# Kernel optimization log

Measured on AMD Instinct MI355X. Metric: run time of the kernel, lower is better.

Reference implementation:

```python
import jax, jax.numpy as jnp
import numpy as np

N_NODE = 50000   # item vocab
D = 100          # embed_dim / hidden_size
N = 49152        # total nodes across all sessions
E = 98304        # edges
B = 4096         # sessions
STDV = 1.0 / np.sqrt(D)


def setup_inputs() -> dict:
    key = jax.random.key(0)
    ks = jax.random.split(key, 20)
    # 1-based item ids, shape [N,1] as in data.x
    x = jax.random.randint(ks[0], (N, 1), 1, N_NODE + 1, dtype=jnp.int32)
    edge_index = jax.random.randint(ks[1], (2, E), 0, N, dtype=jnp.int32)
    # sorted session ids; every session appears at least once (split/nodes[-1] needs non-empty)
    base = jnp.arange(B, dtype=jnp.int32)
    extra = jax.random.randint(ks[2], (N - B,), 0, B, dtype=jnp.int32)
    batch = jnp.sort(jnp.concatenate([base, extra]))

    def u(k, shape):
        return jax.random.uniform(k, shape, minval=-STDV, maxval=STDV, dtype=jnp.float32)

    return {
        "x": x, "edge_index": edge_index, "batch": batch, "num_sessions": B,
        "emb": u(ks[3], (N_NODE, D)),
        "conv_w": u(ks[4], (D, D)),          # GatedGraphConv weight[0]
        "gru_w_ih": u(ks[5], (3 * D, D)),
        "gru_w_hh": u(ks[6], (3 * D, D)),
        "gru_b_ih": u(ks[7], (3 * D,)),
        "gru_b_hh": u(ks[8], (3 * D,)),
        "q_w": u(ks[9], (1, D)), "q_b": u(ks[10], (1,)),
        "w2_w": u(ks[11], (D, D)), "w2_b": u(ks[12], (D,)),
        "w3_w": u(ks[13], (D, D)), "w3_b": u(ks[14], (D,)),
        "w4_w": u(ks[15], (D, 3 * D)), "w4_b": u(ks[16], (D,)),
    }


def _forward(x, edge_index, batch, num_sessions, emb, conv_w,
             gru_w_ih, gru_w_hh, gru_b_ih, gru_b_hh,
             q_w, q_b, w2_w, w2_b, w3_w, w3_b, w4_w, w4_b):
    ids = x[:, 0] - 1                              # data.x - 1
    h0 = emb[ids]                                  # [N, D]

    # GatedGraphConv(num_layers=1): m = x @ W; aggregate sum src->dst; GRUCell update
    src, dst = edge_index[0], edge_index[1]
    m = h0 @ conv_w                                # [N, D]
    agg = jnp.zeros_like(h0).at[dst].add(m[src])   # segment-sum aggregation
    gi = agg @ gru_w_ih.T + gru_b_ih               # [N, 3D]
    gh = h0 @ gru_w_hh.T + gru_b_hh
    i_r, i_z, i_n = jnp.split(gi, 3, axis=1)
    h_r, h_z, h_n = jnp.split(gh, 3, axis=1)
    r = jax.nn.sigmoid(i_r + h_r)
    z = jax.nn.sigmoid(i_z + h_z)
    n = jnp.tanh(i_n + r * h_n)
    xh = jax.nn.relu((1.0 - z) * n + z * h0)       # F.relu(Conv(x, edge_index))

    # last node per session (batch is sorted, sessions non-empty)
    counts = jax.ops.segment_sum(jnp.ones_like(batch), batch, num_segments=num_sessions)
    last_idx = jnp.cumsum(counts) - 1
    v_n = xh[last_idx]                             # [B, D]

    # get_scores: per-session softmax(v_n . nodes) weighted sum -> S_s
    logits = jnp.sum(xh * v_n[batch], axis=1)      # [N]
    mx = jax.ops.segment_max(logits, batch, num_segments=num_sessions)
    p = jnp.exp(logits - mx[batch])
    denom = jax.ops.segment_sum(p, batch, num_segments=num_sessions)
    score = p / denom[batch]                       # [N]
    S_s = jax.ops.segment_sum(score[:, None] * xh, batch, num_segments=num_sessions)

    # sigmoid-gated attention pooling -> S_g
    gate = jax.nn.sigmoid(xh @ w2_w.T + w2_b + v_n[batch] @ w3_w.T + w3_b)
    alpha = gate @ q_w.T + q_b                     # [N, 1]
    S_g = jax.ops.segment_sum(alpha * xh, batch, num_segments=num_sessions)

    S = jnp.concatenate([S_s, S_g, v_n], axis=1) @ w4_w.T + w4_b  # [B, D]
    y_hat = S @ emb.T                              # [B, n_node]
    return y_hat


def reference(x, edge_index, batch, num_sessions, emb, conv_w,
              gru_w_ih, gru_w_hh, gru_b_ih, gru_b_hh,
              q_w, q_b, w2_w, w2_b, w3_w, w3_b, w4_w, w4_b):
    return _forward(x, edge_index, batch, num_sessions, emb, conv_w,
                    gru_w_ih, gru_w_hh, gru_b_ih, gru_b_hh,
                    q_w, q_b, w2_w, w2_b, w3_w, w3_b, w4_w, w4_b)
```

## Files before the change

### kernel.cpp

```cpp
#include <hip/hip_runtime.h>
#include <math.h>

#define DDIM 100
#define PFD  4
#define NTG  4
#define XS   108

using short8 = __attribute__((ext_vector_type(8))) short;
using f32x4  = __attribute__((ext_vector_type(4))) float;


__device__ __forceinline__ float sigm(float x) { return 1.f / (1.f + expf(-x)); }

__device__ __forceinline__ f32x4 mfma16(short8 a, short8 b, f32x4 c) {
  return __builtin_amdgcn_mfma_f32_16x16x32_bf16(a, b, c, 0, 0, 0);
}

__device__ __forceinline__ void gld_lds16(const void* g, void* l) {
  __builtin_amdgcn_global_load_lds(
      (const __attribute__((address_space(1))) void*)g,
      (__attribute__((address_space(3))) void*)l, 16, 0, 0);
}

__device__ __forceinline__ void bf16split(float v, short& h, short& l) {
  unsigned u = __float_as_uint(v);
  unsigned hb = (u + 0x7fffu + ((u >> 16) & 1u)) & 0xffff0000u;
  float res = v - __uint_as_float(hb);
  unsigned u2 = __float_as_uint(res);
  h = (short)(hb >> 16);
  l = (short)((u2 + 0x7fffu + ((u2 >> 16) & 1u)) >> 16);
}

__device__ __forceinline__ short bf16hi(float v) {
  unsigned u = __float_as_uint(v);
  return (short)((u + 0x7fffu + ((u >> 16) & 1u)) >> 16);
}

__global__ __launch_bounds__(256) void k_wc(const float* __restrict__ w_ih,
                                            const float* __restrict__ conv_w,
                                            float* __restrict__ Wc) {
  __shared__ float cwT[100 * 100];
  const int tid = threadIdx.x;
  for (int idx = tid; idx < 10000; idx += 256) {
    int k = idx / 100, t = idx - k * 100;
    cwT[t * 100 + k] = conv_w[idx];
  }
  __syncthreads();
  const int cBase = blockIdx.x * 25;
  for (int o = tid; o < 25 * 100; o += 256) {
    int c = cBase + o / 100;
    int k = o - (o / 100) * 100;
    const float* wr = w_ih + (size_t)c * 100;
    float acc = 0.f;
    for (int t = 0; t < 100; ++t) acc = fmaf(wr[t], cwT[t * 100 + k], acc);
    Wc[(size_t)c * 100 + k] = acc;
  }
}

__global__ void k_packAll(const int* __restrict__ x, const float* __restrict__ emb,
                          const int* __restrict__ batch, const float* __restrict__ Wc,
                          const float* __restrict__ w_hh, const float* __restrict__ w2,
                          const float* __restrict__ w3,
                          short8* __restrict__ Bhi, short8* __restrict__ Blo,
                          short8* __restrict__ Whi,
                          float4* __restrict__ h0, int* __restrict__ last_idx,
                          int NNODE, int NT, int N) {
  int gid = blockIdx.x * 256 + threadIdx.x;
  const int embN = NT * 4 * 64;
  const int wN = 8 * 7 * 4 * 64;
  if (gid < embN) {
    int lane = gid & 63;
    int kt = (gid >> 6) & 3;
    int rt = gid >> 8;
    int r = rt * 16 + (lane & 15);
    if (r >= NNODE) r = NNODE - 1;
    int k0 = kt * 32 + (lane >> 4) * 8;
    float4 f0 = make_float4(0.f, 0.f, 0.f, 0.f);
    float4 f1 = make_float4(0.f, 0.f, 0.f, 0.f);
    if (k0 < 100)     f0 = *(const float4*)(emb + (size_t)r * DDIM + k0);
    if (k0 + 4 < 100) f1 = *(const float4*)(emb + (size_t)r * DDIM + k0 + 4);
    float v[8] = {f0.x, f0.y, f0.z, f0.w, f1.x, f1.y, f1.z, f1.w};
    short8 h, l;
#pragma unroll
    for (int j = 0; j < 8; ++j) {
      short hh, ll;
      bf16split(v[j], hh, ll);
      h[j] = hh; l[j] = ll;
    }
    Bhi[gid] = h;
    Blo[gid] = l;
  } else if (gid < embN + wN) {
    int wg = gid - embN;
    int lane = wg & 63;
    int kt = (wg >> 6) & 3;
    int snt = wg >> 8;
    int nt = snt % 7;
    int s = snt / 7;
    int d = nt * 16 + (lane & 15);
    int k0 = kt * 32 + (lane >> 4) * 8;
    short8 h;
#pragma unroll
    for (int j = 0; j < 8; ++j) {
      int k = k0 + j;
      float v = 0.f;
      if (d < 100 && k < 100) {
        if (s < 3) {
          v = Wc[(size_t)(s * 100 + d) * 100 + k];
        } else if (s < 6) {
          v = w_hh[(size_t)((s - 3) * 100 + d) * 100 + k];
        } else if (s == 6) {
          v = w2[(size_t)d * 100 + k];
        } else {
          v = w3[(size_t)d * 100 + k];
        }
      }
      h[j] = bf16hi(v);
    }
    Whi[wg] = h;
  } else {
    int i = gid - embN - wN;
    if (i < N * 25) {
      int node = i / 25, c = i - node * 25;
      h0[i] = *(const float4*)(emb + (size_t)(x[node] - 1) * DDIM + 4 * c);
    }
    if (i < N) {
      if (i == N - 1 || batch[i + 1] != batch[i]) last_idx[batch[i]] = i;
    }
  }
}

__global__ __launch_bounds__(512, 1) void k_aggregate(
    const int* __restrict__ ei, const float* __restrict__ h0,
    float* __restrict__ aggH, int E) {
  __shared__ float acc[256 * DDIM];
  const int tid = threadIdx.x;
  const int lane = tid & 63;
  const int wave = tid >> 6;
  const int r0 = blockIdx.x * 256;

  for (int idx = tid; idx < 256 * DDIM / 4; idx += 512)
    ((float4*)acc)[idx] = make_float4(0.f, 0.f, 0.f, 0.f);
  __syncthreads();

  const int per = E >> 3;
  const int base = wave * per;
  for (int it = 0; it < per; it += 256) {
    int e0 = base + it + lane * 4;
    int4 d4 = *(const int4*)(ei + E + e0);
    int4 s4 = *(const int4*)(ei + e0);
    int darr[4] = {d4.x, d4.y, d4.z, d4.w};
    int sarr[4] = {s4.x, s4.y, s4.z, s4.w};
#pragma unroll
    for (int j = 0; j < 4; ++j) {
      int dj = darr[j] - r0;
      bool match = (unsigned)dj < 256u;
      unsigned long long mask = __ballot(match);
      while (mask) {
        int bit = __ffsll(mask) - 1;
        mask &= mask - 1;
        int ds = __shfl(dj, bit, 64);
        int ss = __shfl(sarr[j], bit, 64);
        if (lane < 25) {
          float4 v = *(const float4*)(h0 + (size_t)ss * DDIM + 4 * lane);
          float* a = acc + ds * DDIM + 4 * lane;
          atomicAdd(a + 0, v.x); atomicAdd(a + 1, v.y);
          atomicAdd(a + 2, v.z); atomicAdd(a + 3, v.w);
        }
      }
    }
  }
  __syncthreads();
  float4* of = (float4*)(aggH + (size_t)r0 * DDIM);
  for (int idx = tid; idx < 256 * DDIM / 4; idx += 512)
    of[idx] = ((const float4*)acc)[idx];
}

__global__ __launch_bounds__(256) void k_session(
    const float* __restrict__ xh, const float* __restrict__ t2,
    const float* __restrict__ t3v,
    const float* __restrict__ q_w, const float* __restrict__ q_b,
    const int* __restrict__ last_idx, float* __restrict__ Scat, int B) {
  int sid = blockIdx.x * 4 + (threadIdx.x >> 6);
  if (sid >= B) return;
  const int lane = threadIdx.x & 63;
  const int g = lane >> 4;
  const int s = lane & 15;
  const int start = (sid == 0) ? 0 : last_idx[sid - 1] + 1;
  const int end = last_idx[sid];

  float vr[7], t3r[7], qr[7];
#pragma unroll
  for (int k = 0; k < 7; ++k) {
    int c = s + 16 * k;
    bool ok = c < DDIM;
    vr[k]  = ok ? xh[(size_t)end * DDIM + c] : 0.f;
    t3r[k] = ok ? t3v[(size_t)sid * DDIM + c] : 0.f;
    qr[k]  = ok ? q_w[c] : 0.f;
  }
  const float qb = q_b[0];

  float m = -INFINITY, den = 0.f;
  float ss[7] = {}, sg[7] = {};
  for (int i = start; i <= end; i += 4) {
    int ni = i + g;
    bool act = ni <= end;
    int nrow = act ? ni : end;
    float xv[7];
    float l = 0.f, ga = 0.f;
#pragma unroll
    for (int k = 0; k < 7; ++k) {
      int c = s + 16 * k;
      float x = (c < DDIM) ? xh[(size_t)nrow * DDIM + c] : 0.f;
      float tv = (c < DDIM) ? t2[(size_t)nrow * DDIM + c] : 0.f;
      xv[k] = x;
      l = fmaf(x, vr[k], l);
      ga = fmaf(qr[k], sigm(tv + t3r[k]), ga);
    }
#pragma unroll
    for (int o = 1; o <= 8; o <<= 1) {
      l += __shfl_xor(l, o, 64);
      ga += __shfl_xor(ga, o, 64);
    }
    float ls = act ? l : -INFINITY;
    float alpha = act ? (ga + qb) : 0.f;
    float mn = fmaxf(m, ls);
    float cf = (m == -INFINITY) ? 0.f : expf(m - mn);
    float p = act ? expf(ls - mn) : 0.f;
    den = den * cf + p;
#pragma unroll
    for (int k = 0; k < 7; ++k) {
      ss[k] = ss[k] * cf + p * xv[k];
      sg[k] = fmaf(alpha, xv[k], sg[k]);
    }
    m = mn;
  }
  float mAll = m;
  mAll = fmaxf(mAll, __shfl_xor(mAll, 16, 64));
  mAll = fmaxf(mAll, __shfl_xor(mAll, 32, 64));
  float sc = (m == -INFINITY) ? 0.f : expf(m - mAll);
  float dv = den * sc;
  dv += __shfl_xor(dv, 16, 64);
  dv += __shfl_xor(dv, 32, 64);
  float inv = 1.f / dv;
  float* Sc = Scat + (size_t)sid * 300;
#pragma unroll
  for (int k = 0; k < 7; ++k) {
    float sv = ss[k] * sc;
    float gv = sg[k];
    sv += __shfl_xor(sv, 16, 64);  sv += __shfl_xor(sv, 32, 64);
    gv += __shfl_xor(gv, 16, 64);  gv += __shfl_xor(gv, 32, 64);
    int c = s + 16 * k;
    if (g == 0 && c < DDIM) {
      Sc[c] = sv * inv;
      Sc[100 + c] = gv;
      Sc[200 + c] = vr[k];
    }
  }
}

__device__ __forceinline__ void load_afragsH(const float* __restrict__ A, int rowBase,
                                             int lane, short8 ah[4]) {
  int r = rowBase + (lane & 15);
  int g = lane >> 4;
#pragma unroll
  for (int kt = 0; kt < 4; ++kt) {
    int k0 = kt * 32 + g * 8;
    float4 f0 = make_float4(0.f, 0.f, 0.f, 0.f);
    float4 f1 = make_float4(0.f, 0.f, 0.f, 0.f);
    if (k0 < 100)     f0 = *(const float4*)(A + (size_t)r * DDIM + k0);
    if (k0 + 4 < 100) f1 = *(const float4*)(A + (size_t)r * DDIM + k0 + 4);
    short8 h;
    h[0] = bf16hi(f0.x); h[1] = bf16hi(f0.y); h[2] = bf16hi(f0.z); h[3] = bf16hi(f0.w);
    h[4] = bf16hi(f1.x); h[5] = bf16hi(f1.y); h[6] = bf16hi(f1.z); h[7] = bf16hi(f1.w);
    ah[kt] = h;
  }
}

__device__ __forceinline__ void load_afragsHg(const float* __restrict__ A,
                                              const int* __restrict__ idx, int base,
                                              int lane, short8 ah[4]) {
  int r = idx[base + (lane & 15)];
  int g = lane >> 4;
#pragma unroll
  for (int kt = 0; kt < 4; ++kt) {
    int k0 = kt * 32 + g * 8;
    float4 f0 = make_float4(0.f, 0.f, 0.f, 0.f);
    float4 f1 = make_float4(0.f, 0.f, 0.f, 0.f);
    if (k0 < 100)     f0 = *(const float4*)(A + (size_t)r * DDIM + k0);
    if (k0 + 4 < 100) f1 = *(const float4*)(A + (size_t)r * DDIM + k0 + 4);
    short8 h;
    h[0] = bf16hi(f0.x); h[1] = bf16hi(f0.y); h[2] = bf16hi(f0.z); h[3] = bf16hi(f0.w);
    h[4] = bf16hi(f1.x); h[5] = bf16hi(f1.y); h[6] = bf16hi(f1.z); h[7] = bf16hi(f1.w);
    ah[kt] = h;
  }
}

__global__ __launch_bounds__(256) void k_grufused(
    const float* __restrict__ aggH, const float* __restrict__ h0,
    const short8* __restrict__ Whi,
    const float* __restrict__ b_ih, const float* __restrict__ b_hh,
    const float* __restrict__ b2,
    float* __restrict__ xh, float* __restrict__ t2) {
  __shared__ float X[4 * 32 * XS];
  const int lane = threadIdx.x & 63;
  const int wave = threadIdx.x >> 6;
  const int rowBase = blockIdx.x * 128 + wave * 32;
  float* xs = &X[wave * 32 * XS];
  short8 aI0[4], aI1[4], aH0[4], aH1[4];
  load_afragsH(aggH, rowBase, lane, aI0);
  load_afragsH(aggH, rowBase + 16, lane, aI1);
  load_afragsH(h0, rowBase, lane, aH0);
  load_afragsH(h0, rowBase + 16, lane, aH1);
  const int c0 = lane & 15;
  const int r0 = (lane >> 4) * 4;

  for (int nt = 0; nt < 7; ++nt) {
    int d = nt * 16 + c0;
    f32x4 a0[6] = {};
    f32x4 a1[6] = {};
#pragma unroll
    for (int s = 0; s < 6; ++s) {
#pragma unroll
      for (int kt = 0; kt < 4; ++kt) {
        short8 w = Whi[(((size_t)s * 7 + nt) * 4 + kt) * 64 + lane];
        if (s < 3) {
          a0[s] = mfma16(aI0[kt], w, a0[s]);
          a1[s] = mfma16(aI1[kt], w, a1[s]);
        } else {
          a0[s] = mfma16(aH0[kt], w, a0[s]);
          a1[s] = mfma16(aH1[kt], w, a1[s]);
        }
      }
    }
    if (d < 100) {
      float bir = b_ih[d], biz = b_ih[100 + d], bin_ = b_ih[200 + d];
      float bhr = b_hh[d], bhz = b_hh[100 + d], bhn = b_hh[200 + d];
#pragma unroll
      for (int ri = 0; ri < 4; ++ri) {
        {
          int row = rowBase + r0 + ri;
          float r = sigm(a0[0][ri] + bir + a0[3][ri] + bhr);
          float z = sigm(a0[1][ri] + biz + a0[4][ri] + bhz);
          float n = tanhf(a0[2][ri] + bin_ + r * (a0[5][ri] + bhn));
          float h0v = h0[(size_t)row * DDIM + d];
          float v = (1.f - z) * n + z * h0v;
          xs[(r0 + ri) * XS + d] = v > 0.f ? v : 0.f;
        }
        {
          int row = rowBase + 16 + r0 + ri;
          float r = sigm(a1[0][ri] + bir + a1[3][ri] + bhr);
          float z = sigm(a1[1][ri] + biz + a1[4][ri] + bhz);
          float n = tanhf(a1[2][ri] + bin_ + r * (a1[5][ri] + bhn));
          float h0v = h0[(size_t)row * DDIM + d];
          float v = (1.f - z) * n + z * h0v;
          xs[(16 + r0 + ri) * XS + d] = v > 0.f ? v : 0.f;
        }
      }
    }
  }

  const int lr = lane / 25;
  const int lc4 = (lane - lr * 25) * 4;
  if (lane < 50) {
#pragma unroll
    for (int p = 0; p < 16; ++p) {
      int row = p * 2 + lr;
      f32x4 v = *(const f32x4*)&xs[row * XS + lc4];
      *(f32x4*)(xh + (size_t)(rowBase + row) * DDIM + lc4) = v;
    }
  }

  short8 xa0[4], xa1[4];
  {
    int r = lane & 15;
    int g = lane >> 4;
#pragma unroll
    for (int kt = 0; kt < 4; ++kt) {
      int k0 = kt * 32 + g * 8;
      short8 h0f, h1f;
#pragma unroll
      for (int j = 0; j < 8; ++j) {
        int k = k0 + j;
        float v0 = (k < 100) ? xs[r * XS + k] : 0.f;
        float v1 = (k < 100) ? xs[(16 + r) * XS + k] : 0.f;
        h0f[j] = bf16hi(v0);
        h1f[j] = bf16hi(v1);
      }
      xa0[kt] = h0f;
      xa1[kt] = h1f;
    }
  }

  for (int nt = 0; nt < 7; ++nt) {
    int d = nt * 16 + c0;
    f32x4 ac0 = {0.f, 0.f, 0.f, 0.f};
    f32x4 ac1 = {0.f, 0.f, 0.f, 0.f};
#pragma unroll
    for (int kt = 0; kt < 4; ++kt) {
      short8 w = Whi[(((size_t)6 * 7 + nt) * 4 + kt) * 64 + lane];
      ac0 = mfma16(xa0[kt], w, ac0);
      ac1 = mfma16(xa1[kt], w, ac1);
    }
    if (d < 100) {
      float b = b2[d];
#pragma unroll
      for (int ri = 0; ri < 4; ++ri) {
        xs[(r0 + ri) * XS + d] = ac0[ri] + b;
        xs[(16 + r0 + ri) * XS + d] = ac1[ri] + b;
      }
    }
  }
  if (lane < 50) {
#pragma unroll
    for (int p = 0; p < 16; ++p) {
      int row = p * 2 + lr;
      f32x4 v = *(const f32x4*)&xs[row * XS + lc4];
      *(f32x4*)(t2 + (size_t)(rowBase + row) * DDIM + lc4) = v;
    }
  }
}

__global__ __launch_bounds__(256) void k_t3v(
    const float* __restrict__ xh, const short8* __restrict__ Whi,
    const float* __restrict__ b3, const int* __restrict__ lastI,
    float* __restrict__ t3v) {
  const int lane = threadIdx.x & 63;
  const int wave = threadIdx.x >> 6;
  const int rowBase = blockIdx.x * 128 + wave * 32;
  short8 a0[4], a1[4];
  load_afragsHg(xh, lastI, rowBase, lane, a0);
  load_afragsHg(xh, lastI, rowBase + 16, lane, a1);
  const int c0 = lane & 15;
  const int r0 = (lane >> 4) * 4;

  for (int nt = 0; nt < 7; ++nt) {
    int d = nt * 16 + c0;
    f32x4 ac0 = {0.f, 0.f, 0.f, 0.f};
    f32x4 ac1 = {0.f, 0.f, 0.f, 0.f};
#pragma unroll
    for (int kt = 0; kt < 4; ++kt) {
      short8 w = Whi[(((size_t)7 * 7 + nt) * 4 + kt) * 64 + lane];
      ac0 = mfma16(a0[kt], w, ac0);
      ac1 = mfma16(a1[kt], w, ac1);
    }
    if (d < 100) {
      float b = b3[d];
#pragma unroll
      for (int ri = 0; ri < 4; ++ri) {
        t3v[(size_t)(rowBase + r0 + ri) * DDIM + d] = ac0[ri] + b;
        t3v[(size_t)(rowBase + 16 + r0 + ri) * DDIM + d] = ac1[ri] + b;
      }
    }
  }
}

__global__ __launch_bounds__(256, 2) void k_gemmS(
    const float* __restrict__ A, const float* __restrict__ Bm,
    const float* __restrict__ bias, short* __restrict__ Ph, short* __restrict__ Pl,
    int M) {
  __shared__ float4 As4[25 * 128];
  __shared__ float4 Bs4[25 * 64];
  const int m0 = blockIdx.y * 128;
  const int n0 = blockIdx.x * 64;
  const int t = threadIdx.x;
  const int tx = t & 15;
  const int ty = t >> 4;
  float acc[8][4] = {};

  for (int kt = 0; kt < 300; kt += 100) {
    for (int idx = t; idx < 128 * 25; idx += 256) {
      int r = idx / 25, k4 = idx - r * 25;
      int ar = m0 + r; if (ar >= M) ar = M - 1;
      float4 v = *(const float4*)(A + (size_t)ar * 300 + kt + 4 * k4);
      As4[k4 * 128 + (r ^ (k4 & 7))] = v;
    }
    for (int idx = t; idx < 64 * 25; idx += 256) {
      int r = idx / 25, k4 = idx - r * 25;
      int br = n0 + r;
      float4 v = make_float4(0.f, 0.f, 0.f, 0.f);
      if (br < 100) v = *(const float4*)(Bm + (size_t)br * 300 + kt + 4 * k4);
      Bs4[k4 * 64 + (r ^ (k4 & 7))] = v;
    }
    __syncthreads();
#pragma unroll 5
    for (int k4 = 0; k4 < 25; ++k4) {
      const int s = k4 & 7;
      float4 av[8], bv[4];
#pragma unroll
      for (int i = 0; i < 8; ++i) av[i] = As4[k4 * 128 + ((ty + 16 * i) ^ s)];
#pragma unroll
      for (int j = 0; j < 4; ++j) bv[j] = Bs4[k4 * 64 + ((tx + 16 * j) ^ s)];
#pragma unroll
      for (int i = 0; i < 8; ++i) {
#pragma unroll
        for (int j = 0; j < 4; ++j) {
          acc[i][j] = fmaf(av[i].x, bv[j].x, acc[i][j]);
          acc[i][j] = fmaf(av[i].y, bv[j].y, acc[i][j]);
          acc[i][j] = fmaf(av[i].z, bv[j].z, acc[i][j]);
          acc[i][j] = fmaf(av[i].w, bv[j].w, acc[i][j]);
        }
      }
    }
    __syncthreads();
  }

#pragma unroll
  for (int i = 0; i < 8; ++i) {
    int row = m0 + ty + 16 * i;
    if (row >= M) continue;
#pragma unroll
    for (int j = 0; j < 4; ++j) {
      int col = n0 + tx + 16 * j;
      float v = (col < 100) ? (acc[i][j] + bias[col]) : 0.f;
      short hh, ll;
      bf16split(v, hh, ll);
      int rt = row >> 4, kt = col >> 5;
      int lane_t = (row & 15) + 16 * ((col >> 3) & 3);
      size_t base = ((((size_t)rt * 4 + kt) * 64 + lane_t) << 3) + (col & 7);
      Ph[base] = hh;
      Pl[base] = ll;
    }
  }
}

__global__ __launch_bounds__(256) void k_bigmm(
    const short8* __restrict__ Ahi, const short8* __restrict__ Alo,
    const short8* __restrict__ Bhi, const short8* __restrict__ Blo,
    float* __restrict__ out, int NT, int NTCHUNK, int NCOLS) {
  __shared__ short8 Bs[PFD * 8 * 64];
  __shared__ float Xp[4 * 32 * 64];
  const int lane = threadIdx.x & 63;
  const int wave = threadIdx.x >> 6;
  const int mt0 = blockIdx.x * 8 + wave * 2;

  short8 ah[2][4], al[2][4];
#pragma unroll
  for (int mi = 0; mi < 2; ++mi)
#pragma unroll
    for (int kt = 0; kt < 4; ++kt) {
      size_t off = ((size_t)(mt0 + mi) * 4 + kt) * 64 + lane;
      ah[mi][kt] = Ahi[off];
      al[mi][kt] = Alo[off];
    }

  const int nt0 = blockIdx.y * NTCHUNK;
  const int nt1 = min(NT, nt0 + NTCHUNK);
  const int r0 = (lane >> 4) * 4;
  const int c0 = lane & 15;
  float* xp = &Xp[wave * 32 * 64];

  auto issueB = [&](int nt) {
    int s = nt & (PFD - 1);
    gld_lds16(Bhi + ((size_t)nt * 4 + wave) * 64 + lane, &Bs[(s * 8 + wave) * 64]);
    gld_lds16(Blo + ((size_t)nt * 4 + wave) * 64 + lane, &Bs[(s * 8 + 4 + wave) * 64]);
  };

  for (int i = 0; i < PFD && nt0 + i < nt1; ++i) issueB(nt0 + i);
  asm volatile("s_waitcnt vmcnt(6)" ::: "memory");
  __builtin_amdgcn_s_barrier();

  for (int g = nt0; g < nt1; g += NTG) {
    const int jn = min(NTG, nt1 - g);
    f32x4 acc[2][NTG] = {};
#pragma unroll
    for (int j = 0; j < NTG; ++j) {
      if (j >= jn) break;
      const int nt = g + j;
      const int s = nt & (PFD - 1);
      short8 bh[4], bl[4];
#pragma unroll
      for (int kt = 0; kt < 4; ++kt) {
        bh[kt] = Bs[(s * 8 + kt) * 64 + lane];
        bl[kt] = Bs[(s * 8 + 4 + kt) * 64 + lane];
      }
      asm volatile("s_waitcnt lgkmcnt(0)" ::: "memory");
      __builtin_amdgcn_s_barrier();
      if (nt + PFD < nt1) issueB(nt + PFD);
      __builtin_amdgcn_sched_barrier(0);
#pragma unroll
      for (int kt = 0; kt < 4; ++kt) {
        acc[0][j] = mfma16(ah[0][kt], bh[kt], acc[0][j]);
        acc[1][j] = mfma16(ah[1][kt], bh[kt], acc[1][j]);
        acc[0][j] = mfma16(ah[0][kt], bl[kt], acc[0][j]);
        acc[1][j] = mfma16(ah[1][kt], bl[kt], acc[1][j]);
        acc[0][j] = mfma16(al[0][kt], bh[kt], acc[0][j]);
        acc[1][j] = mfma16(al[1][kt], bh[kt], acc[1][j]);
      }
      asm volatile("s_waitcnt vmcnt(14)" ::: "memory");
      __builtin_amdgcn_s_barrier();
    }
#pragma unroll
    for (int mi = 0; mi < 2; ++mi)
#pragma unroll
      for (int j = 0; j < NTG; ++j) {
        if (j < jn) {
#pragma unroll
          for (int r = 0; r < 4; ++r) {
            int rl = mi * 16 + r0 + r;
            int cl = j * 16 + c0;
            xp[rl * 64 + (cl ^ (((rl >> 2) & 3) << 4))] = acc[mi][j][r];
          }
        }
      }
    const int colbase = g * 16;
#pragma unroll
    for (int it = 0; it < 8; ++it) {
      int rl = it * 4 + (lane >> 4);
      int cl = 4 * c0;
      if (cl < jn * 16) {
        f32x4 v = *(const f32x4*)&xp[rl * 64 + (cl ^ (((rl >> 2) & 3) << 4))];
        int row = mt0 * 16 + rl;
        __builtin_nontemporal_store(v, (f32x4*)(out + (size_t)row * NCOLS + colbase + cl));
      }
    }
  }
}


extern "C" void kernel_launch(void* const* d_in, const int* in_sizes, int n_in,
                              void* d_out, int out_size, void* d_ws, size_t ws_size,
                              hipStream_t stream) {
  const int*   x      = (const int*)d_in[0];
  const int*   ei     = (const int*)d_in[1];
  const int*   batch  = (const int*)d_in[2];
  const float* emb    = (const float*)d_in[4];
  const float* conv_w = (const float*)d_in[5];
  const float* w_ih   = (const float*)d_in[6];
  const float* w_hh   = (const float*)d_in[7];
  const float* b_ih   = (const float*)d_in[8];
  const float* b_hh   = (const float*)d_in[9];
  const float* q_w    = (const float*)d_in[10];
  const float* q_b    = (const float*)d_in[11];
  const float* w2     = (const float*)d_in[12];
  const float* b2     = (const float*)d_in[13];
  const float* w3     = (const float*)d_in[14];
  const float* b3     = (const float*)d_in[15];
  const float* w4     = (const float*)d_in[16];
  const float* b4     = (const float*)d_in[17];

  const int N = in_sizes[0];
  const int E = in_sizes[1] / 2;
  const int NNODE = in_sizes[4] / DDIM;
  const int B = out_size / NNODE;

  size_t ND = (size_t)N * DDIM;
  float* ws   = (float*)d_ws;
  float* h0   = ws;
  float* aggH = ws + ND;
  float* xh   = ws + 2 * ND;
  float* t2   = ws + 3 * ND;
  float* aux  = ws + 4 * ND;
  float* t3v  = aux;
  float* Scat = t3v + (size_t)B * DDIM;
  int*   lastI = (int*)(Scat + 3 * (size_t)B * DDIM);

  const int MT = (B + 15) / 16;
  const int NT = (NNODE + 15) / 16;
  short8* Whi = (short8*)(lastI + B);
  short8* Ahi = Whi + 8 * 7 * 4 * 64;
  short8* Alo = Ahi + (size_t)MT * 4 * 64;
  short8* Bhi = Alo + (size_t)MT * 4 * 64;
  short8* Blo = Bhi + (size_t)NT * 4 * 64;
  float*  Wc  = (float*)(Blo + (size_t)NT * 4 * 64);

  dim3 blk(256);
  const int nblkA = N / 128;
  const int nblkB = B / 128;

  int packTotal = NT * 4 * 64 + 8 * 7 * 4 * 64 + N * 25;
  k_wc<<<12, blk, 0, stream>>>(w_ih, conv_w, Wc);
  k_packAll<<<(packTotal + 255) / 256, blk, 0, stream>>>(
      x, emb, batch, Wc, w_hh, w2, w3, Bhi, Blo, Whi,
      (float4*)h0, lastI, NNODE, NT, N);
  k_aggregate<<<N / 256, dim3(512), 0, stream>>>(ei, h0, aggH, E);
  k_grufused<<<nblkA, blk, 0, stream>>>(aggH, h0, Whi, b_ih, b_hh, b2, xh, t2);
  k_t3v<<<nblkB, blk, 0, stream>>>(xh, Whi, b3, lastI, t3v);
  k_session<<<(B + 3) / 4, blk, 0, stream>>>(xh, t2, t3v, q_w, q_b, lastI, Scat, B);
  k_gemmS<<<dim3(2, B / 128), blk, 0, stream>>>(Scat, w4, b4, (short*)Ahi, (short*)Alo, B);

  const int NTCHUNK = 48;
  const int NCHUNKS = (NT + NTCHUNK - 1) / NTCHUNK;
  k_bigmm<<<dim3(nblkB, NCHUNKS), blk, 0, stream>>>(
      Ahi, Alo, Bhi, Blo, (float*)d_out, NT, NTCHUNK, NNODE);
}
```

Before: 404.3 us.

## Fuse edge aggregation with GRU update and drop materialized h0 gather

Merges the scatter-add aggregation kernel with the GRU/gate kernel so the aggregated features stay in shared memory instead of round-tripping through a global aggH buffer. The packed h0 gather is removed; embedding rows are read directly via x indices in both the aggregation and the GRU stage. This saves two N×D global writes and reads plus one launch. The cost is an extra indirect x lookup per edge inside the atomic loop, and the GRU phase now runs at one 512-thread block per CU with no overlap.

```diff
diff --git a/kernel.cpp b/kernel.cpp
--- a/kernel.cpp
+++ b/kernel.cpp
@@ -4,7 +4,6 @@
 #define DDIM 100
 #define PFD  4
 #define NTG  4
-#define XS   108
 
 using short8 = __attribute__((ext_vector_type(8))) short;
 using f32x4  = __attribute__((ext_vector_type(4))) float;
@@ -57,13 +56,12 @@
   }
 }
 
-__global__ void k_packAll(const int* __restrict__ x, const float* __restrict__ emb,
-                          const int* __restrict__ batch, const float* __restrict__ Wc,
+__global__ void k_packAll(const int* __restrict__ batch, const float* __restrict__ emb,
+                          const float* __restrict__ Wc,
                           const float* __restrict__ w_hh, const float* __restrict__ w2,
                           const float* __restrict__ w3,
                           short8* __restrict__ Bhi, short8* __restrict__ Blo,
-                          short8* __restrict__ Whi,
-                          float4* __restrict__ h0, int* __restrict__ last_idx,
+                          short8* __restrict__ Whi, int* __restrict__ last_idx,
                           int NNODE, int NT, int N) {
   int gid = blockIdx.x * 256 + threadIdx.x;
   const int embN = NT * 4 * 64;
@@ -104,39 +102,33 @@
       int k = k0 + j;
       float v = 0.f;
       if (d < 100 && k < 100) {
-        if (s < 3) {
-          v = Wc[(size_t)(s * 100 + d) * 100 + k];
-        } else if (s < 6) {
-          v = w_hh[(size_t)((s - 3) * 100 + d) * 100 + k];
-        } else if (s == 6) {
-          v = w2[(size_t)d * 100 + k];
-        } else {
-          v = w3[(size_t)d * 100 + k];
-        }
+        if (s < 3)      v = Wc[(size_t)(s * 100 + d) * 100 + k];
+        else if (s < 6) v = w_hh[(size_t)((s - 3) * 100 + d) * 100 + k];
+        else if (s == 6) v = w2[(size_t)d * 100 + k];
+        else             v = w3[(size_t)d * 100 + k];
       }
       h[j] = bf16hi(v);
     }
     Whi[wg] = h;
   } else {
     int i = gid - embN - wN;
-    if (i < N * 25) {
-      int node = i / 25, c = i - node * 25;
-      h0[i] = *(const float4*)(emb + (size_t)(x[node] - 1) * DDIM + 4 * c);
-    }
     if (i < N) {
       if (i == N - 1 || batch[i + 1] != batch[i]) last_idx[batch[i]] = i;
     }
   }
 }
 
-__global__ __launch_bounds__(512, 1) void k_aggregate(
-    const int* __restrict__ ei, const float* __restrict__ h0,
-    float* __restrict__ aggH, int E) {
+__global__ __launch_bounds__(512, 1) void k_aggGru(
+    const int* __restrict__ ei, const int* __restrict__ x,
+    const float* __restrict__ emb, const short8* __restrict__ Whi,
+    const float* __restrict__ b_ih, const float* __restrict__ b_hh,
+    const float* __restrict__ b2,
+    float* __restrict__ xh, float* __restrict__ t2, int E) {
   __shared__ float acc[256 * DDIM];
   const int tid = threadIdx.x;
   const int lane = tid & 63;
   const int wave = tid >> 6;
-  const int r0 = blockIdx.x * 256;
+  const int r0blk = blockIdx.x * 256;
 
   for (int idx = tid; idx < 256 * DDIM / 4; idx += 512)
     ((float4*)acc)[idx] = make_float4(0.f, 0.f, 0.f, 0.f);
@@ -152,7 +144,7 @@
     int sarr[4] = {s4.x, s4.y, s4.z, s4.w};
 #pragma unroll
     for (int j = 0; j < 4; ++j) {
-      int dj = darr[j] - r0;
+      int dj = darr[j] - r0blk;
       bool match = (unsigned)dj < 256u;
       unsigned long long mask = __ballot(match);
       while (mask) {
@@ -161,7 +153,8 @@
         int ds = __shfl(dj, bit, 64);
         int ss = __shfl(sarr[j], bit, 64);
         if (lane < 25) {
-          float4 v = *(const float4*)(h0 + (size_t)ss * DDIM + 4 * lane);
+          int er = x[ss] - 1;
+          float4 v = *(const float4*)(emb + (size_t)er * DDIM + 4 * lane);
           float* a = acc + ds * DDIM + 4 * lane;
           atomicAdd(a + 0, v.x); atomicAdd(a + 1, v.y);
           atomicAdd(a + 2, v.z); atomicAdd(a + 3, v.w);
@@ -170,9 +163,171 @@
     }
   }
   __syncthreads();
-  float4* of = (float4*)(aggH + (size_t)r0 * DDIM);
-  for (int idx = tid; idx < 256 * DDIM / 4; idx += 512)
-    of[idx] = ((const float4*)acc)[idx];
+
+  const int lr = wave * 32;
+  const int rowBase = r0blk + lr;
+  const int c0 = lane & 15;
+  const int rq = (lane >> 4) * 4;
+
+  short8 aI0[4], aI1[4];
+  {
+    int r = lane & 15;
+    int g = lane >> 4;
+#pragma unroll
+    for (int kt = 0; kt < 4; ++kt) {
+      int k0 = kt * 32 + g * 8;
+      short8 h0f, h1f;
+#pragma unroll
+      for (int j = 0; j < 8; ++j) {
+        int k = k0 + j;
+        float v0 = (k < 100) ? acc[(lr + r) * DDIM + k] : 0.f;
+        float v1 = (k < 100) ? acc[(lr + 16 + r) * DDIM + k] : 0.f;
+        h0f[j] = bf16hi(v0);
+        h1f[j] = bf16hi(v1);
+      }
+      aI0[kt] = h0f;
+      aI1[kt] = h1f;
+    }
+  }
+  short8 aH0[4], aH1[4];
+  {
+    int r0g = x[rowBase + (lane & 15)] - 1;
+    int r1g = x[rowBase + 16 + (lane & 15)] - 1;
+    int g = lane >> 4;
+#pragma unroll
+    for (int kt = 0; kt < 4; ++kt) {
+      int k0 = kt * 32 + g * 8;
+      float4 a0f = make_float4(0.f, 0.f, 0.f, 0.f), a1f = a0f;
+      float4 b0f = a0f, b1f = a0f;
+      if (k0 < 100) {
+        a0f = *(const float4*)(emb + (size_t)r0g * DDIM + k0);
+        b0f = *(const float4*)(emb + (size_t)r1g * DDIM + k0);
+      }
+      if (k0 + 4 < 100) {
+        a1f = *(const float4*)(emb + (size_t)r0g * DDIM + k0 + 4);
+        b1f = *(const float4*)(emb + (size_t)r1g * DDIM + k0 + 4);
+      }
+      float v0[8] = {a0f.x, a0f.y, a0f.z, a0f.w, a1f.x, a1f.y, a1f.z, a1f.w};
+      float v1[8] = {b0f.x, b0f.y, b0f.z, b0f.w, b1f.x, b1f.y, b1f.z, b1f.w};
+      short8 h0f, h1f;
+#pragma unroll
+      for (int j = 0; j < 8; ++j) {
+        h0f[j] = bf16hi(v0[j]);
+        h1f[j] = bf16hi(v1[j]);
+      }
+      aH0[kt] = h0f;
+      aH1[kt] = h1f;
+    }
+  }
+  int xr0[4], xr1[4];
+#pragma unroll
+  for (int ri = 0; ri < 4; ++ri) {
+    xr0[ri] = x[rowBase + rq + ri] - 1;
+    xr1[ri] = x[rowBase + 16 + rq + ri] - 1;
+  }
+
+  for (int nt = 0; nt < 7; ++nt) {
+    int d = nt * 16 + c0;
+    f32x4 a0[6] = {};
+    f32x4 a1[6] = {};
+#pragma unroll
+    for (int s = 0; s < 6; ++s) {
+#pragma unroll
+      for (int kt = 0; kt < 4; ++kt) {
+        short8 w = Whi[(((size_t)s * 7 + nt) * 4 + kt) * 64 + lane];
+        if (s < 3) {
+          a0[s] = mfma16(aI0[kt], w, a0[s]);
+          a1[s] = mfma16(aI1[kt], w, a1[s]);
+        } else {
+          a0[s] = mfma16(aH0[kt], w, a0[s]);
+          a1[s] = mfma16(aH1[kt], w, a1[s]);
+        }
+      }
+    }
+    if (d < 100) {
+      float bir = b_ih[d], biz = b_ih[100 + d], bin_ = b_ih[200 + d];
+      float bhr = b_hh[d], bhz = b_hh[100 + d], bhn = b_hh[200 + d];
+#pragma unroll
+      for (int ri = 0; ri < 4; ++ri) {
+        {
+          float r = sigm(a0[0][ri] + bir + a0[3][ri] + bhr);
+          float z = sigm(a0[1][ri] + biz + a0[4][ri] + bhz);
+          float n = tanhf(a0[2][ri] + bin_ + r * (a0[5][ri] + bhn));
+          float h0v = emb[(size_t)xr0[ri] * DDIM + d];
+          float v = (1.f - z) * n + z * h0v;
+          acc[(lr + rq + ri) * DDIM + d] = v > 0.f ? v : 0.f;
+        }
+        {
+          float r = sigm(a1[0][ri] + bir + a1[3][ri] + bhr);
+          float z = sigm(a1[1][ri] + biz + a1[4][ri] + bhz);
+          float n = tanhf(a1[2][ri] + bin_ + r * (a1[5][ri] + bhn));
+          float h0v = emb[(size_t)xr1[ri] * DDIM + d];
+          float v = (1.f - z) * n + z * h0v;
+          acc[(lr + 16 + rq + ri) * DDIM + d] = v > 0.f ? v : 0.f;
+        }
+      }
+    }
+  }
+
+  const int dr = lane / 25;
+  const int dc4 = (lane - dr * 25) * 4;
+  if (lane < 50) {
+#pragma unroll
+    for (int p = 0; p < 16; ++p) {
+      int row = p * 2 + dr;
+      f32x4 v = *(const f32x4*)&acc[(lr + row) * DDIM + dc4];
+      *(f32x4*)(xh + (size_t)(rowBase + row) * DDIM + dc4) = v;
+    }
+  }
+
+  short8 xa0[4], xa1[4];
+  {
+    int r = lane & 15;
+    int g = lane >> 4;
+#pragma unroll
+    for (int kt = 0; kt < 4; ++kt) {
+      int k0 = kt * 32 + g * 8;
+      short8 h0f, h1f;
+#pragma unroll
+      for (int j = 0; j < 8; ++j) {
+        int k = k0 + j;
+        float v0 = (k < 100) ? acc[(lr + r) * DDIM + k] : 0.f;
+        float v1 = (k < 100) ? acc[(lr + 16 + r) * DDIM + k] : 0.f;
+        h0f[j] = bf16hi(v0);
+        h1f[j] = bf16hi(v1);
+      }
+      xa0[kt] = h0f;
+      xa1[kt] = h1f;
+    }
+  }
+
+  for (int nt = 0; nt < 7; ++nt) {
+    int d = nt * 16 + c0;
+    f32x4 ac0 = {0.f, 0.f, 0.f, 0.f};
+    f32x4 ac1 = {0.f, 0.f, 0.f, 0.f};
+#pragma unroll
+    for (int kt = 0; kt < 4; ++kt) {
+      short8 w = Whi[(((size_t)6 * 7 + nt) * 4 + kt) * 64 + lane];
+      ac0 = mfma16(xa0[kt], w, ac0);
+      ac1 = mfma16(xa1[kt], w, ac1);
+    }
+    if (d < 100) {
+      float b = b2[d];
+#pragma unroll
+      for (int ri = 0; ri < 4; ++ri) {
+        acc[(lr + rq + ri) * DDIM + d] = ac0[ri] + b;
+        acc[(lr + 16 + rq + ri) * DDIM + d] = ac1[ri] + b;
+      }
+    }
+  }
+  if (lane < 50) {
+#pragma unroll
+    for (int p = 0; p < 16; ++p) {
+      int row = p * 2 + dr;
+      f32x4 v = *(const f32x4*)&acc[(lr + row) * DDIM + dc4];
+      *(f32x4*)(t2 + (size_t)(rowBase + row) * DDIM + dc4) = v;
+    }
+  }
 }
 
 __global__ __launch_bounds__(256) void k_session(
@@ -258,9 +413,10 @@
   }
 }
 
-__device__ __forceinline__ void load_afragsH(const float* __restrict__ A, int rowBase,
-                                             int lane, short8 ah[4]) {
-  int r = rowBase + (lane & 15);
+__device__ __forceinline__ void load_afragsHg(const float* __restrict__ A,
+                                              const int* __restrict__ idx, int base,
+                                              int lane, short8 ah[4]) {
+  int r = idx[base + (lane & 15)];
   int g = lane >> 4;
 #pragma unroll
   for (int kt = 0; kt < 4; ++kt) {
@@ -273,150 +429,6 @@
     h[0] = bf16hi(f0.x); h[1] = bf16hi(f0.y); h[2] = bf16hi(f0.z); h[3] = bf16hi(f0.w);
     h[4] = bf16hi(f1.x); h[5] = bf16hi(f1.y); h[6] = bf16hi(f1.z); h[7] = bf16hi(f1.w);
     ah[kt] = h;
-  }
-}
-
-__device__ __forceinline__ void load_afragsHg(const float* __restrict__ A,
-                                              const int* __restrict__ idx, int base,
-                                              int lane, short8 ah[4]) {
-  int r = idx[base + (lane & 15)];
-  int g = lane >> 4;
-#pragma unroll
-  for (int kt = 0; kt < 4; ++kt) {
-    int k0 = kt * 32 + g * 8;
-    float4 f0 = make_float4(0.f, 0.f, 0.f, 0.f);
-    float4 f1 = make_float4(0.f, 0.f, 0.f, 0.f);
-    if (k0 < 100)     f0 = *(const float4*)(A + (size_t)r * DDIM + k0);
-    if (k0 + 4 < 100) f1 = *(const float4*)(A + (size_t)r * DDIM + k0 + 4);
-    short8 h;
-    h[0] = bf16hi(f0.x); h[1] = bf16hi(f0.y); h[2] = bf16hi(f0.z); h[3] = bf16hi(f0.w);
-    h[4] = bf16hi(f1.x); h[5] = bf16hi(f1.y); h[6] = bf16hi(f1.z); h[7] = bf16hi(f1.w);
-    ah[kt] = h;
-  }
-}
-
-__global__ __launch_bounds__(256) void k_grufused(
-    const float* __restrict__ aggH, const float* __restrict__ h0,
-    const short8* __restrict__ Whi,
-    const float* __restrict__ b_ih, const float* __restrict__ b_hh,
-    const float* __restrict__ b2,
-    float* __restrict__ xh, float* __restrict__ t2) {
-  __shared__ float X[4 * 32 * XS];
-  const int lane = threadIdx.x & 63;
-  const int wave = threadIdx.x >> 6;
-  const int rowBase = blockIdx.x * 128 + wave * 32;
-  float* xs = &X[wave * 32 * XS];
-  short8 aI0[4], aI1[4], aH0[4], aH1[4];
-  load_afragsH(aggH, rowBase, lane, aI0);
-  load_afragsH(aggH, rowBase + 16, lane, aI1);
-  load_afragsH(h0, rowBase, lane, aH0);
-  load_afragsH(h0, rowBase + 16, lane, aH1);
-  const int c0 = lane & 15;
-  const int r0 = (lane >> 4) * 4;
-
-  for (int nt = 0; nt < 7; ++nt) {
-    int d = nt * 16 + c0;
-    f32x4 a0[6] = {};
-    f32x4 a1[6] = {};
-#pragma unroll
-    for (int s = 0; s < 6; ++s) {
-#pragma unroll
-      for (int kt = 0; kt < 4; ++kt) {
-        short8 w = Whi[(((size_t)s * 7 + nt) * 4 + kt) * 64 + lane];
-        if (s < 3) {
-          a0[s] = mfma16(aI0[kt], w, a0[s]);
-          a1[s] = mfma16(aI1[kt], w, a1[s]);
-        } else {
-          a0[s] = mfma16(aH0[kt], w, a0[s]);
-          a1[s] = mfma16(aH1[kt], w, a1[s]);
-        }
-      }
-    }
-    if (d < 100) {
-      float bir = b_ih[d], biz = b_ih[100 + d], bin_ = b_ih[200 + d];
-      float bhr = b_hh[d], bhz = b_hh[100 + d], bhn = b_hh[200 + d];
-#pragma unroll
-      for (int ri = 0; ri < 4; ++ri) {
-        {
-          int row = rowBase + r0 + ri;
-          float r = sigm(a0[0][ri] + bir + a0[3][ri] + bhr);
-          float z = sigm(a0[1][ri] + biz + a0[4][ri] + bhz);
-          float n = tanhf(a0[2][ri] + bin_ + r * (a0[5][ri] + bhn));
-          float h0v = h0[(size_t)row * DDIM + d];
-          float v = (1.f - z) * n + z * h0v;
-          xs[(r0 + ri) * XS + d] = v > 0.f ? v : 0.f;
-        }
-        {
-          int row = rowBase + 16 + r0 + ri;
-          float r = sigm(a1[0][ri] + bir + a1[3][ri] + bhr);
-          float z = sigm(a1[1][ri] + biz + a1[4][ri] + bhz);
-          float n = tanhf(a1[2][ri] + bin_ + r * (a1[5][ri] + bhn));
-          float h0v = h0[(size_t)row * DDIM + d];
-          float v = (1.f - z) * n + z * h0v;
-          xs[(16 + r0 + ri) * XS + d] = v > 0.f ? v : 0.f;
-        }
-      }
-    }
-  }
-
-  const int lr = lane / 25;
-  const int lc4 = (lane - lr * 25) * 4;
-  if (lane < 50) {
-#pragma unroll
-    for (int p = 0; p < 16; ++p) {
-      int row = p * 2 + lr;
-      f32x4 v = *(const f32x4*)&xs[row * XS + lc4];
-      *(f32x4*)(xh + (size_t)(rowBase + row) * DDIM + lc4) = v;
-    }
-  }
-
-  short8 xa0[4], xa1[4];
-  {
-    int r = lane & 15;
-    int g = lane >> 4;
-#pragma unroll
-    for (int kt = 0; kt < 4; ++kt) {
-      int k0 = kt * 32 + g * 8;
-      short8 h0f, h1f;
-#pragma unroll
-      for (int j = 0; j < 8; ++j) {
-        int k = k0 + j;
-        float v0 = (k < 100) ? xs[r * XS + k] : 0.f;
-        float v1 = (k < 100) ? xs[(16 + r) * XS + k] : 0.f;
-        h0f[j] = bf16hi(v0);
-        h1f[j] = bf16hi(v1);
-      }
-      xa0[kt] = h0f;
-      xa1[kt] = h1f;
-    }
-  }
-
-  for (int nt = 0; nt < 7; ++nt) {
-    int d = nt * 16 + c0;
-    f32x4 ac0 = {0.f, 0.f, 0.f, 0.f};
-    f32x4 ac1 = {0.f, 0.f, 0.f, 0.f};
-#pragma unroll
-    for (int kt = 0; kt < 4; ++kt) {
-      short8 w = Whi[(((size_t)6 * 7 + nt) * 4 + kt) * 64 + lane];
-      ac0 = mfma16(xa0[kt], w, ac0);
-      ac1 = mfma16(xa1[kt], w, ac1);
-    }
-    if (d < 100) {
-      float b = b2[d];
-#pragma unroll
-      for (int ri = 0; ri < 4; ++ri) {
-        xs[(r0 + ri) * XS + d] = ac0[ri] + b;
-        xs[(16 + r0 + ri) * XS + d] = ac1[ri] + b;
-      }
-    }
-  }
-  if (lane < 50) {
-#pragma unroll
-    for (int p = 0; p < 16; ++p) {
-      int row = p * 2 + lr;
-      f32x4 v = *(const f32x4*)&xs[row * XS + lc4];
-      *(f32x4*)(t2 + (size_t)(rowBase + row) * DDIM + lc4) = v;
-    }
   }
 }
 
@@ -645,11 +657,9 @@
 
   size_t ND = (size_t)N * DDIM;
   float* ws   = (float*)d_ws;
-  float* h0   = ws;
-  float* aggH = ws + ND;
-  float* xh   = ws + 2 * ND;
-  float* t2   = ws + 3 * ND;
-  float* aux  = ws + 4 * ND;
+  float* xh   = ws;
+  float* t2   = ws + ND;
+  float* aux  = ws + 2 * ND;
   float* t3v  = aux;
   float* Scat = t3v + (size_t)B * DDIM;
   int*   lastI = (int*)(Scat + 3 * (size_t)B * DDIM);
@@ -664,16 +674,14 @@
   float*  Wc  = (float*)(Blo + (size_t)NT * 4 * 64);
 
   dim3 blk(256);
-  const int nblkA = N / 128;
   const int nblkB = B / 128;
 
-  int packTotal = NT * 4 * 64 + 8 * 7 * 4 * 64 + N * 25;
+  int packTotal = NT * 4 * 64 + 8 * 7 * 4 * 64 + N;
   k_wc<<<12, blk, 0, stream>>>(w_ih, conv_w, Wc);
   k_packAll<<<(packTotal + 255) / 256, blk, 0, stream>>>(
-      x, emb, batch, Wc, w_hh, w2, w3, Bhi, Blo, Whi,
-      (float4*)h0, lastI, NNODE, NT, N);
-  k_aggregate<<<N / 256, dim3(512), 0, stream>>>(ei, h0, aggH, E);
-  k_grufused<<<nblkA, blk, 0, stream>>>(aggH, h0, Whi, b_ih, b_hh, b2, xh, t2);
+      batch, emb, Wc, w_hh, w2, w3, Bhi, Blo, Whi, lastI, NNODE, NT, N);
+  k_aggGru<<<N / 256, dim3(512), 0, stream>>>(ei, x, emb, Whi, b_ih, b_hh, b2,
+                                              xh, t2, E);
   k_t3v<<<nblkB, blk, 0, stream>>>(xh, Whi, b3, lastI, t3v);
   k_session<<<(B + 3) / 4, blk, 0, stream>>>(xh, t2, t3v, q_w, q_b, lastI, Scat, B);
   k_gemmS<<<dim3(2, B / 128), blk, 0, stream>>>(Scat, w4, b4, (short*)Ahi, (short*)Alo, B);
```

Measured after the change: 394.2 us. -2.5%, faster.
